# Kernel optimization log

Hardware: AMD Instinct MI355X
Metric: run time of the kernel (lower is better)

The kernel has to match this reference:

```python
import jax, jax.numpy as jnp
import numpy as np

MASS = 60.0


def setup_inputs() -> dict:
    key = jax.random.key(0)
    k1, k2, k3 = jax.random.split(key, 3)
    pre_len, batch, n_nb = 64, 1024, 256
    output = jax.random.normal(k1, (pre_len, batch, 2), dtype=jnp.float32)
    target = jax.random.normal(k2, (pre_len, batch, 2), dtype=jnp.float32)
    # neighbours: [batch, n_nb, 5] = [coord_x, coord_y, v_x, v_y, angle]
    neighbours = jax.random.normal(k3, (batch, n_nb, 5), dtype=jnp.float32)
    return {"output": output, "target": target, "neighbours": neighbours}


def _field_energy(out_bt2, neighbours):
    # out_bt2: [B, T, 2]; neighbours: [B, N, 5]
    nx = neighbours[:, None, :, 0]   # [B, 1, N]
    ny = neighbours[:, None, :, 1]
    ang = neighbours[:, None, :, 4]
    px = out_bt2[:, :, 0][:, :, None]  # [B, T, 1]
    py = out_bt2[:, :, 1][:, :, None]
    dx = px - nx                     # [B, T, N]
    dy = py - ny
    ca, sa = jnp.cos(ang), jnp.sin(ang)
    x_ = ca * dx + sa * dy
    y_ = -sa * dx + ca * dy
    energy_i = MASS / (x_ ** 6 + y_ ** 6 + 6.0)  # [B, T, N]
    nb_angle = jnp.arctan2(-dy, -dx)             # atan2(ny - py, nx - px)
    ex = jnp.sum(energy_i * jnp.cos(nb_angle), axis=-1)  # [B, T]
    ey = jnp.sum(energy_i * jnp.sin(nb_angle), axis=-1)
    energy_norm = jnp.sqrt(ex ** 2 + ey ** 2)    # [B, T]
    # mean over prediction steps per pedestrian, then mean over pedestrians
    return jnp.mean(jnp.mean(energy_norm, axis=1))


def reference(output, target, neighbours):
    loss1 = jnp.mean((output - target) ** 2)  # nn.MSELoss default
    out_bt2 = jnp.transpose(output, (1, 0, 2))  # [B, T, 2]
    field_energy_mean = _field_energy(out_bt2, neighbours)
    return loss1 + field_energy_mean
```

## Files before the change

### kernel.cpp

```cpp
#include <hip/hip_runtime.h>
#include <math.h>

#define PRE_LEN 64
#define BATCH   1024
#define NNB     256

typedef float v2f __attribute__((ext_vector_type(2)));

__global__ __launch_bounds__(512, 4) void field_loss_stage1(
    const float* __restrict__ output,
    const float* __restrict__ target,
    const float* __restrict__ nbr,
    float* __restrict__ ws)
{
    __shared__ float4 s_nb[2][NNB];
    __shared__ float4 s_red[2][4][32];

    const int tid = threadIdx.x;
    const int l   = tid & 63;
    const int q   = tid >> 6;
    const int g   = q >> 2;
    const int qg  = q & 3;
    const int p   = l & 31;
    const int t0  = 2 * p;
    const int b   = 2 * blockIdx.x + g;

    const size_t o0 = (size_t)t0 * (BATCH * 2) + (size_t)b * 2;
    const size_t o1 = o0 + (BATCH * 2);
    const float2 a0 = *reinterpret_cast<const float2*>(&output[o0]);
    const float2 a1 = *reinterpret_cast<const float2*>(&output[o1]);
    float2 tg0 = make_float2(0.f, 0.f), tg1 = make_float2(0.f, 0.f);
    if (qg == 0) {
        tg0 = *reinterpret_cast<const float2*>(&target[o0]);
        tg1 = *reinterpret_cast<const float2*>(&target[o1]);
    }

    {
        const int gs = tid >> 8;
        const int n  = tid & 255;
        const float* pn = nbr + (((size_t)(2 * blockIdx.x + gs)) * NNB + n) * 5;
        const float nx  = pn[0];
        const float ny  = pn[1];
        const float ang = pn[4];
        const float rev = ang * 0.31830988618f;
        const float c2  = __builtin_amdgcn_cosf(rev);
        const float s2  = __builtin_amdgcn_sinf(rev);
        s_nb[gs][n] = make_float4(nx, ny, c2, 0.5f * s2);
    }
    __syncthreads();

    const v2f px = { a0.x, a1.x };
    const v2f py = { a0.y, a1.y };

    v2f ex = 0.0f, ey = 0.0f;
    const int n0 = ((l >> 5) + 2 * qg) * 32;
#pragma unroll 8
    for (int i = 0; i < 32; ++i) {
        const float4 nb = s_nb[g][n0 + i];
        const v2f dx  = px - nb.x;
        const v2f dy  = py - nb.y;
        const v2f dx2 = dx * dx;
        const v2f pp  = dx * dy;
        const v2f r2  = __builtin_elementwise_fma(dy, dy, dx2);
        const v2f qq  = __builtin_elementwise_fma(dy, -dy, dx2);
        const v2f xy  = __builtin_elementwise_fma(pp, (v2f)nb.z, -(qq * nb.w));
        const v2f inr = __builtin_elementwise_fma(xy * -3.0f, xy, r2 * r2);
        const v2f den = __builtin_elementwise_fma(r2, inr, (v2f)6.0f);
        const v2f m2  = den * den * r2;
        const v2f s   = { __builtin_amdgcn_rsqf(m2.x),
                          __builtin_amdgcn_rsqf(m2.y) };
        ex = __builtin_elementwise_fma(s, dx, ex);
        ey = __builtin_elementwise_fma(s, dy, ey);
    }

    float ex0 = ex.x + __shfl_xor(ex.x, 32, 64);
    float ey0 = ey.x + __shfl_xor(ey.x, 32, 64);
    float ex1 = ex.y + __shfl_xor(ex.y, 32, 64);
    float ey1 = ey.y + __shfl_xor(ey.y, 32, 64);

    if (l < 32)
        s_red[g][qg][p] = make_float4(ex0, ey0, ex1, ey1);
    __syncthreads();

    if (qg == 0) {
        float tex0 = 0.0f, tey0 = 0.0f, tex1 = 0.0f, tey1 = 0.0f;
        #pragma unroll
        for (int k = 0; k < 4; ++k) {
            const float4 r = s_red[g][k][p];
            tex0 += r.x; tey0 += r.y; tex1 += r.z; tey1 += r.w;
        }
        const float en0 = __builtin_amdgcn_sqrtf(
            __builtin_fmaf(tex0, tex0, tey0 * tey0));
        const float en1 = __builtin_amdgcn_sqrtf(
            __builtin_fmaf(tex1, tex1, tey1 * tey1));

        const float d0x = a0.x - tg0.x, d0y = a0.y - tg0.y;
        const float d1x = a1.x - tg1.x, d1y = a1.y - tg1.y;

        float val = (en0 + en1) * (60.0f / (PRE_LEN * BATCH))
                  + (d0x * d0x + d0y * d0y + d1x * d1x + d1y * d1y)
                    * (1.0f / (PRE_LEN * BATCH * 2));

        #pragma unroll
        for (int off = 16; off > 0; off >>= 1)
            val += __shfl_down(val, off, 64);

        if (l == 0)
            ws[b] = val;
    }
}

__global__ __launch_bounds__(64) void reduce_kernel(
    const float4* __restrict__ ws4,
    float* __restrict__ out)
{
    const int l = threadIdx.x;
    const float4 a = ws4[l];
    const float4 b = ws4[l + 64];
    const float4 c = ws4[l + 128];
    const float4 d = ws4[l + 192];
    float v = ((a.x + a.y) + (a.z + a.w)) + ((b.x + b.y) + (b.z + b.w))
            + ((c.x + c.y) + (c.z + c.w)) + ((d.x + d.y) + (d.z + d.w));

    #pragma unroll
    for (int off = 32; off > 0; off >>= 1)
        v += __shfl_down(v, off, 64);

    if (l == 0)
        out[0] = v;
}

extern "C" void kernel_launch(void* const* d_in, const int* in_sizes, int n_in,
                              void* d_out, int out_size, void* d_ws, size_t ws_size,
                              hipStream_t stream) {
    const float* output = (const float*)d_in[0];
    const float* target = (const float*)d_in[1];
    const float* nbr    = (const float*)d_in[2];
    float* out = (float*)d_out;
    float* ws  = (float*)d_ws;

    field_loss_stage1<<<dim3(BATCH / 2), dim3(512), 0, stream>>>(output, target, nbr, ws);
    reduce_kernel<<<dim3(1), dim3(64), 0, stream>>>((const float4*)ws, out);
}
```

Baseline: 14.55 us.

## Fuse final reduction via atomicAdd and process four pedestrians per block

Drops the second reduce kernel: each block now sums its partial results in shared memory and atomically adds one value to the output, which is zeroed by a memset beforehand. Blocks grow to 1024 threads covering four batch entries, halving the grid. This removes one kernel launch and the workspace round trip, but adds a memset launch and makes the float summation order nondeterministic. The larger blocks may also reduce occupancy flexibility.

```diff
diff --git a/kernel.cpp b/kernel.cpp
--- a/kernel.cpp
+++ b/kernel.cpp
@@ -7,14 +7,15 @@
 
 typedef float v2f __attribute__((ext_vector_type(2)));
 
-__global__ __launch_bounds__(512, 4) void field_loss_stage1(
+__global__ __launch_bounds__(1024, 4) void field_loss_fused(
     const float* __restrict__ output,
     const float* __restrict__ target,
     const float* __restrict__ nbr,
-    float* __restrict__ ws)
+    float* __restrict__ out)
 {
-    __shared__ float4 s_nb[2][NNB];
-    __shared__ float4 s_red[2][4][32];
+    __shared__ float4 s_nb[4][NNB];
+    __shared__ float4 s_red[4][4][32];
+    __shared__ float  s_sum[4];
 
     const int tid = threadIdx.x;
     const int l   = tid & 63;
@@ -23,7 +24,7 @@
     const int qg  = q & 3;
     const int p   = l & 31;
     const int t0  = 2 * p;
-    const int b   = 2 * blockIdx.x + g;
+    const int b   = 4 * blockIdx.x + g;
 
     const size_t o0 = (size_t)t0 * (BATCH * 2) + (size_t)b * 2;
     const size_t o1 = o0 + (BATCH * 2);
@@ -38,7 +39,7 @@
     {
         const int gs = tid >> 8;
         const int n  = tid & 255;
-        const float* pn = nbr + (((size_t)(2 * blockIdx.x + gs)) * NNB + n) * 5;
+        const float* pn = nbr + (((size_t)(4 * blockIdx.x + gs)) * NNB + n) * 5;
         const float nx  = pn[0];
         const float ny  = pn[1];
         const float ang = pn[4];
@@ -73,10 +74,10 @@
         ey = __builtin_elementwise_fma(s, dy, ey);
     }
 
-    float ex0 = ex.x + __shfl_xor(ex.x, 32, 64);
-    float ey0 = ey.x + __shfl_xor(ey.x, 32, 64);
-    float ex1 = ex.y + __shfl_xor(ex.y, 32, 64);
-    float ey1 = ey.y + __shfl_xor(ey.y, 32, 64);
+    const float ex0 = ex.x + __shfl_xor(ex.x, 32, 64);
+    const float ey0 = ey.x + __shfl_xor(ey.x, 32, 64);
+    const float ex1 = ex.y + __shfl_xor(ex.y, 32, 64);
+    const float ey1 = ey.y + __shfl_xor(ey.y, 32, 64);
 
     if (l < 32)
         s_red[g][qg][p] = make_float4(ex0, ey0, ex1, ey1);
@@ -106,28 +107,12 @@
             val += __shfl_down(val, off, 64);
 
         if (l == 0)
-            ws[b] = val;
+            s_sum[g] = val;
     }
-}
+    __syncthreads();
 
-__global__ __launch_bounds__(64) void reduce_kernel(
-    const float4* __restrict__ ws4,
-    float* __restrict__ out)
-{
-    const int l = threadIdx.x;
-    const float4 a = ws4[l];
-    const float4 b = ws4[l + 64];
-    const float4 c = ws4[l + 128];
-    const float4 d = ws4[l + 192];
-    float v = ((a.x + a.y) + (a.z + a.w)) + ((b.x + b.y) + (b.z + b.w))
-            + ((c.x + c.y) + (c.z + c.w)) + ((d.x + d.y) + (d.z + d.w));
-
-    #pragma unroll
-    for (int off = 32; off > 0; off >>= 1)
-        v += __shfl_down(v, off, 64);
-
-    if (l == 0)
-        out[0] = v;
+    if (tid == 0)
+        atomicAdd(out, (s_sum[0] + s_sum[1]) + (s_sum[2] + s_sum[3]));
 }
 
 extern "C" void kernel_launch(void* const* d_in, const int* in_sizes, int n_in,
@@ -137,8 +122,8 @@
     const float* target = (const float*)d_in[1];
     const float* nbr    = (const float*)d_in[2];
     float* out = (float*)d_out;
-    float* ws  = (float*)d_ws;
 
-    field_loss_stage1<<<dim3(BATCH / 2), dim3(512), 0, stream>>>(output, target, nbr, ws);
-    reduce_kernel<<<dim3(1), dim3(64), 0, stream>>>((const float4*)ws, out);
+    hipMemsetAsync(out, 0, sizeof(float), stream);
+    field_loss_fused<<<dim3(BATCH / 4), dim3(1024), 0, stream>>>(
+        output, target, nbr, out);
 }
```

New measurement: 21.32 us. 1.47x slower.
